# Optimization experiments

Measured on AMD Instinct MI355X. Metric: run time of the kernel, lower is better.

Reference implementation:

```python
import jax, jax.numpy as jnp
import numpy as np

EPS = 1e-06


def setup_inputs() -> dict:
    key = jax.random.key(0)
    k1, k2, k3 = jax.random.split(key, 3)
    N, L, H, D = 2, 2048, 8, 64
    return {
        "queries": jax.random.normal(k1, (N, L, H, D), dtype=jnp.float32),
        "keys": jax.random.normal(k2, (N, L, H, D), dtype=jnp.float32),
        "values": jax.random.normal(k3, (N, L, H, D), dtype=jnp.float32),
    }


def reference(queries, keys, values):
    # [N, L, H, D] -> [N, H, L, D]
    q = jnp.transpose(queries, (0, 2, 1, 3))
    k = jnp.transpose(keys, (0, 2, 1, 3))
    v = jnp.transpose(values, (0, 2, 1, 3))
    # kernel_method = sigmoid (applied to q and k only)
    q = jax.nn.sigmoid(q)
    k = jax.nn.sigmoid(k)
    L = q.shape[2]
    normal = (jnp.arange(L, dtype=q.dtype) + 1.0)[None, None, :]  # [1,1,L]

    sink_incoming = 1.0 / jnp.einsum('nhld,nhld->nhl', q + EPS, jnp.cumsum(k, axis=2) + EPS)
    source_outgoing = 1.0 / jnp.einsum('nhld,nhld->nhl', k + EPS, jnp.cumsum(q, axis=2) + EPS)
    sink_incoming = sink_incoming * normal
    source_outgoing = source_outgoing * normal

    conserved_sink = jnp.einsum(
        'nhld,nhld->nhl', q + EPS,
        jnp.cumsum(k * source_outgoing[..., None], axis=2) + EPS) / normal
    conserved_source = jnp.einsum(
        'nhld,nhld->nhl', k + EPS,
        jnp.cumsum(q * sink_incoming[..., None], axis=2) + EPS) / normal
    conserved_source = jnp.clip(conserved_source, -1.0, 1.0)

    sink_allocation = jax.nn.sigmoid(conserved_sink)
    conserved_source = jnp.exp(conserved_source)
    source_competition = conserved_source / jnp.cumsum(conserved_source, axis=-1) * normal

    # causal dot product: outer-product cumsum as in the original
    q_scaled = q * (sink_incoming / normal)[..., None]
    v_scaled = v * source_competition[..., None]
    kv = jnp.cumsum(jnp.einsum('nhld,nhlm->nhldm', k, v_scaled), axis=2)  # [N,H,L,D,M]
    qkv = jnp.einsum('nhld,nhldm->nhlm', q_scaled, kv)
    x = qkv * sink_allocation[..., None]
    # back to [N, L, H, M]
    return jnp.transpose(x, (0, 2, 1, 3))
```

## Files before the change

kernel.cpp:

```cpp
#include <hip/hip_runtime.h>
#include <math.h>

constexpr int Nn = 2, Hh = 8, Ll = 2048, Dd = 64;
constexpr int S  = Nn * Hh;
constexpr int C  = 64;
constexpr int NC = Ll / C;
constexpr int SC = S * NC;

constexpr int SB  = 72;
constexpr int SRP = 65;
constexpr int SS8 = 9;

#define EPSF 1e-6f
#define FLAG_MAGIC 0x5F3A9D21u

typedef __attribute__((ext_vector_type(8))) short short8;
typedef __attribute__((ext_vector_type(4))) float f32x4;
#define MFMA16(a, b, c) __builtin_amdgcn_mfma_f32_16x16x32_bf16(a, b, c, 0, 0, 0)

__device__ __forceinline__ float rcpf(float x) { return __builtin_amdgcn_rcpf(x); }
__device__ __forceinline__ float sigf(float x) { return rcpf(1.0f + __expf(-x)); }

__device__ __forceinline__ float waveRed(float v) {
#pragma unroll
    for (int off = 32; off > 0; off >>= 1) v += __shfl_xor(v, off, 64);
    return v;
}

__device__ __forceinline__ int gidx(int n, int l, int h, int d) {
    return ((n * Ll + l) * Hh + h) * Dd + d;
}

__device__ __forceinline__ float fc(const float4& v, int u) { return ((const float*)&v)[u]; }

__device__ __forceinline__ unsigned short f2bf(float x) {
    unsigned int u = __float_as_uint(x);
    unsigned int r = (u + 0x7fffu + ((u >> 16) & 1u)) >> 16;
    return (unsigned short)r;
}
__device__ __forceinline__ unsigned int pack2(float lo, float hi) {
    return (unsigned int)f2bf(lo) | ((unsigned int)f2bf(hi) << 16);
}
__device__ __forceinline__ float bf2f(unsigned short u) {
    return __uint_as_float(((unsigned int)u) << 16);
}
__device__ __forceinline__ float lo16(unsigned int x) { return __uint_as_float(x << 16); }
__device__ __forceinline__ float hi16(unsigned int x) { return __uint_as_float(x & 0xffff0000u); }
__device__ __forceinline__ void unpack8(const uint4& v, float* o) {
    o[0] = lo16(v.x); o[1] = hi16(v.x); o[2] = lo16(v.y); o[3] = hi16(v.y);
    o[4] = lo16(v.z); o[5] = hi16(v.z); o[6] = lo16(v.w); o[7] = hi16(v.w);
}

__device__ __forceinline__ void pubf(float* p, float v) {
    __hip_atomic_store((unsigned int*)p, __float_as_uint(v),
                       __ATOMIC_RELAXED, __HIP_MEMORY_SCOPE_AGENT);
}
__device__ __forceinline__ float rdf(const float* p) {
    return __uint_as_float(__hip_atomic_load((const unsigned int*)p,
                       __ATOMIC_RELAXED, __HIP_MEMORY_SCOPE_AGENT));
}
__device__ __forceinline__ void publish_flag(unsigned int* f, int t) {
    asm volatile("s_waitcnt vmcnt(0)" ::: "memory");
    __syncthreads();
    if (t == 0)
        __hip_atomic_store(f, FLAG_MAGIC, __ATOMIC_RELAXED, __HIP_MEMORY_SCOPE_AGENT);
}
__device__ __forceinline__ void wait_flags(const unsigned int* fbase, int s, int c, int t) {
    if (t < 64) {
        const bool need = (t < c);
        for (;;) {
            unsigned int v = need
                ? __hip_atomic_load(&fbase[s * NC + t], __ATOMIC_RELAXED, __HIP_MEMORY_SCOPE_AGENT)
                : FLAG_MAGIC;
            if (__all(v == FLAG_MAGIC)) break;
            __builtin_amdgcn_s_sleep(8);
        }
    }
    __syncthreads();
}

__global__ __launch_bounds__(256) void k_mega(
        const float* __restrict__ Q, const float* __restrict__ K,
        const float* __restrict__ V,
        unsigned short* __restrict__ Qb, unsigned short* __restrict__ Kb,
        unsigned short* __restrict__ Vt,
        float* __restrict__ SK, float* __restrict__ SQ,
        float* __restrict__ SKso, float* __restrict__ SQsi,
        float* __restrict__ s2_g, float* __restrict__ scomp_g,
        float* __restrict__ Tcs, float* __restrict__ KVT,
        unsigned int* __restrict__ f0, unsigned int* __restrict__ f1,
        unsigned int* __restrict__ f2) {
    __shared__ __align__(16) unsigned short sqB[C * SB];
    __shared__ __align__(16) unsigned short skB[C * SB];
    __shared__ __align__(16) unsigned short vsT[C * SB];
    __shared__ float P[C * SRP];
    __shared__ float scrA[C * SS8], scrB[C * SS8];
    __shared__ float colK[C], colQ[C], pk[Dd], pq[Dd];
    __shared__ float lsi[C], lso[C], rw1[C], rw2[C], le[C], ecum[C], lsc[C];
    __shared__ float pcsv;

    const int b = blockIdx.x, s = b / NC, c = b % NC;
    const int n = s / Hh, h = s % Hh, t = threadIdx.x;
    const size_t base = (size_t)b * 4096;

    {
        int d0 = (4 * t) & 63, ig = t >> 4;
        float psk[4] = {0, 0, 0, 0}, psq[4] = {0, 0, 0, 0};
#pragma unroll
        for (int j = 0; j < 4; j++) {
            int i = ig + 16 * j;
            int id = gidx(n, c * C + i, h, d0);
            float4 q4 = *(const float4*)&Q[id];
            float4 k4 = *(const float4*)&K[id];
            float a0 = sigf(q4.x), a1 = sigf(q4.y), a2 = sigf(q4.z), a3 = sigf(q4.w);
            float b0 = sigf(k4.x), b1 = sigf(k4.y), b2 = sigf(k4.z), b3 = sigf(k4.w);
            uint2 pq2 = make_uint2(pack2(a0, a1), pack2(a2, a3));
            uint2 pk2 = make_uint2(pack2(b0, b1), pack2(b2, b3));
            *(uint2*)&Qb[base + i * 64 + d0] = pq2;
            *(uint2*)&Kb[base + i * 64 + d0] = pk2;
            *(uint2*)&sqB[i * SB + d0] = pq2;
            *(uint2*)&skB[i * SB + d0] = pk2;
            psq[0] += a0; psq[1] += a1; psq[2] += a2; psq[3] += a3;
            psk[0] += b0; psk[1] += b1; psk[2] += b2; psk[3] += b3;
        }
#pragma unroll
        for (int r = 0; r < 4; r++) {
            P[ig * 64 + d0 + r] = psk[r];
            P[1024 + ig * 64 + d0 + r] = psq[r];
        }
        int i0 = (t & 15) * 4, dt = (t >> 4) * 4;
        float4 vr[4];
#pragma unroll
        for (int r = 0; r < 4; r++)
            vr[r] = *(const float4*)&V[gidx(n, c * C + i0 + r, h, dt)];
#pragma unroll
        for (int u = 0; u < 4; u++) {
            uint2 wv = make_uint2(pack2(fc(vr[0], u), fc(vr[1], u)),
                                  pack2(fc(vr[2], u), fc(vr[3], u)));
            *(uint2*)&Vt[base + (dt + u) * 64 + i0] = wv;
            *(uint2*)&vsT[(dt + u) * SB + i0] = wv;
        }
    }
    __syncthreads();
    if (t < 64) {
        float v = 0.f;
        for (int g = 0; g < 16; g++) v += P[g * 64 + t];
        pubf(&SK[b * 64 + t], v);
    } else if (t < 128) {
        int d = t - 64; float v = 0.f;
        for (int g = 0; g < 16; g++) v += P[1024 + g * 64 + d];
        pubf(&SQ[b * 64 + d], v);
    }
    publish_flag(&f0[b], t);

    wait_flags(f0, s, c, t);

    {
        int d = t & 63, g = t >> 6;
        float pa = 0.f, pb = 0.f;
        for (int cp = g; cp < c; cp += 4) {
            pa += rdf(&SK[(s * NC + cp) * 64 + d]);
            pb += rdf(&SQ[(s * NC + cp) * 64 + d]);
        }
        P[2048 + g * 64 + d] = pa;
        P[2304 + g * 64 + d] = pb;
    }
#pragma unroll
    for (int j = 0; j < 2; j++) {
        int flat = 8 * t + 2048 * j, i = flat >> 6, d0 = flat & 63;
        uint4 xq = *(const uint4*)&sqB[i * SB + d0];
        uint4 xk = *(const uint4*)&skB[i * SB + d0];
        float qa[8], ka[8];
        unpack8(xq, qa); unpack8(xk, ka);
        float sq = 0.f, sk = 0.f;
#pragma unroll
        for (int u = 0; u < 8; u++) { sq += qa[u]; sk += ka[u]; }
        scrB[i * SS8 + (d0 >> 3)] = sq;
        scrA[i * SS8 + (d0 >> 3)] = sk;
    }
    __syncthreads();
    if (t < 64) {
        float v = 0.f;
#pragma unroll
        for (int u = 0; u < 8; u++) v += scrA[t * SS8 + u];
        colK[t] = v;
    } else if (t < 128) {
        int i = t - 64; float v = 0.f;
#pragma unroll
        for (int u = 0; u < 8; u++) v += scrB[i * SS8 + u];
        colQ[i] = v;
    } else if (t < 192) {
        int d = t - 128;
        pk[d] = P[2048 + d] + P[2112 + d] + P[2176 + d] + P[2240 + d];
    } else {
        int d = t - 192;
        pq[d] = P[2304 + d] + P[2368 + d] + P[2432 + d] + P[2496 + d];
    }
    __syncthreads();

    {
        int w = t >> 6, lane = t & 63, m = lane & 15, q = lane >> 4;
        f32x4 acc[4] = {{0,0,0,0},{0,0,0,0},{0,0,0,0},{0,0,0,0}};
#pragma unroll
        for (int kk = 0; kk < 64; kk += 32) {
            short8 a = *(const short8*)&sqB[(16 * w + m) * SB + kk + q * 8];
#pragma unroll
            for (int J = 0; J < 4; J++) {
                short8 bb = *(const short8*)&skB[(16 * J + m) * SB + kk + q * 8];
                acc[J] = MFMA16(a, bb, acc[J]);
            }
        }
#pragma unroll
        for (int J = 0; J < 4; J++)
#pragma unroll
            for (int r = 0; r < 4; r++)
                P[(16 * w + 4 * q + r) * SRP + 16 * J + m] = acc[J][r];
    }
    __syncthreads();

    {
        int i = t >> 2, g = t & 3, l = c * C + i;
        float r1 = 0.f, r2 = 0.f;
        for (int jj = g; jj <= i; jj += 4) {
            r1 += P[i * SRP + jj] + EPSF * colK[jj];
            r2 += P[jj * SRP + i] + EPSF * colQ[jj];
        }
        float b1 = 0.f, b2 = 0.f;
#pragma unroll
        for (int u = 0; u < 16; u++) {
            int d = g * 16 + u;
            b1 += (bf2f(sqB[i * SB + d]) + EPSF) * (pk[d] + EPSF);
            b2 += (bf2f(skB[i * SB + d]) + EPSF) * (pq[d] + EPSF);
        }
        r1 += __shfl_xor(r1, 1, 64); r1 += __shfl_xor(r1, 2, 64);
        r2 += __shfl_xor(r2, 1, 64); r2 += __shfl_xor(r2, 2, 64);
        b1 += __shfl_xor(b1, 1, 64); b1 += __shfl_xor(b1, 2, 64);
        b2 += __shfl_xor(b2, 1, 64); b2 += __shfl_xor(b2, 2, 64);
        if (g == 0) {
            float nf = (float)(l + 1);
            lsi[i] = nf * rcpf(b1 + r1);
            lso[i] = nf * rcpf(b2 + r2);
        }
    }
    __syncthreads();

    {
        int i = t >> 2, g = t & 3;
        float a1 = 0.f, a2 = 0.f;
        for (int jj = g; jj <= i; jj += 4) {
            a1 += lso[jj] * (P[i * SRP + jj] + EPSF * colK[jj]);
            a2 += lsi[jj] * (P[jj * SRP + i] + EPSF * colQ[jj]);
        }
        a1 += __shfl_xor(a1, 1, 64); a1 += __shfl_xor(a1, 2, 64);
        a2 += __shfl_xor(a2, 1, 64); a2 += __shfl_xor(a2, 2, 64);
        if (g == 0) { rw1[i] = a1; rw2[i] = a2; }
    }
    {
        int d = t >> 2, g = t & 3;
        float v1 = 0.f, v2 = 0.f;
#pragma unroll
        for (int u = 0; u < 16; u++) {
            int i = g * 16 + u;
            v1 += bf2f(skB[i * SB + d]) * lso[i];
            v2 += bf2f(sqB[i * SB + d]) * lsi[i];
        }
        v1 += __shfl_xor(v1, 1, 64); v1 += __shfl_xor(v1, 2, 64);
        v2 += __shfl_xor(v2, 1, 64); v2 += __shfl_xor(v2, 2, 64);
        if (g == 0) {
            pubf(&SKso[b * 64 + d], v1);
            pubf(&SQsi[b * 64 + d], v2);
        }
    }
    publish_flag(&f1[b], t);

    wait_flags(f1, s, c, t);

    {
        int d = t & 63, g = t >> 6;
        float pa = 0.f, pb = 0.f;
        for (int cp = g; cp < c; cp += 4) {
            pa += rdf(&SKso[(s * NC + cp) * 64 + d]);
            pb += rdf(&SQsi[(s * NC + cp) * 64 + d]);
        }
        scrA[g * 64 + d] = pa;
        scrA[256 + g * 64 + d] = pb;
    }
    __syncthreads();
    if (t < 64) pk[t] = scrA[t] + scrA[64 + t] + scrA[128 + t] + scrA[192 + t];
    else if (t < 128) {
        int d = t - 64;
        pq[d] = scrA[256 + d] + scrA[320 + d] + scrA[384 + d] + scrA[448 + d];
    }
    __syncthreads();
    {
        int i = t >> 2, g = t & 3, l = c * C + i;
        float b1 = 0.f, b2 = 0.f;
#pragma unroll
        for (int j = 0; j < 2; j++) {
            uint4 xq = *(const uint4*)&sqB[i * SB + g * 16 + 8 * j];
            uint4 xk = *(const uint4*)&skB[i * SB + g * 16 + 8 * j];
            float qa[8], ka[8];
            unpack8(xq, qa); unpack8(xk, ka);
            int d = g * 16 + 8 * j;
#pragma unroll
            for (int u = 0; u < 8; u++) {
                b1 += (qa[u] + EPSF) * (pk[d + u] + EPSF);
                b2 += (ka[u] + EPSF) * (pq[d + u] + EPSF);
            }
        }
        b1 += __shfl_xor(b1, 1, 64); b1 += __shfl_xor(b1, 2, 64);
        b2 += __shfl_xor(b2, 1, 64); b2 += __shfl_xor(b2, 2, 64);
        if (g == 0) {
            float nf = (float)(l + 1);
            float cs  = (b1 + rw1[i]) * rcpf(nf);
            float csr = (b2 + rw2[i]) * rcpf(nf);
            csr = fminf(fmaxf(csr, -1.f), 1.f);
            float e = __expf(csr);
            float sal = sigf(cs);
            s2_g[s * Ll + l] = lsi[i] * rcpf(nf) * sal;
            le[i] = e;
        }
    }
    __syncthreads();
    if (t < 64) {
        float run = le[t];
#pragma unroll
        for (int off = 1; off < 64; off <<= 1) {
            float o = __shfl_up(run, off, 64);
            if (t >= off) run += o;
        }
        ecum[t] = run;
        if (t == 63) pubf(&Tcs[b], run);
    }
    publish_flag(&f2[b], t);

    wait_flags(f2, s, c, t);

    if (t < 64) {
        float v = (t < c) ? rdf(&Tcs[s * NC + t]) : 0.f;
        v = waveRed(v);
        if (t == 0) pcsv = v;
    }
    __syncthreads();
    if (t < 64) {
        int l = c * C + t;
        float ls = le[t] * rcpf(pcsv + ecum[t]) * (float)(l + 1);
        lsc[t] = ls;
        scomp_g[s * Ll + l] = ls;
    }
    __syncthreads();

    unsigned short* skT = (unsigned short*)P;
#pragma unroll
    for (int j = 0; j < 2; j++) {
        int flat = 8 * t + 2048 * j, dR = flat >> 6, i0 = flat & 63;
        uint4 vv = *(const uint4*)&vsT[dR * SB + i0];
        float x[8];
        unpack8(vv, x);
#pragma unroll
        for (int u = 0; u < 8; u++) x[u] *= lsc[i0 + u];
        uint4 o;
        o.x = pack2(x[0], x[1]); o.y = pack2(x[2], x[3]);
        o.z = pack2(x[4], x[5]); o.w = pack2(x[6], x[7]);
        *(uint4*)&vsT[dR * SB + i0] = o;
    }
    {
        int i0 = (t & 15) * 4, dt = (t >> 4) * 4;
        uint2 kr[4];
#pragma unroll
        for (int r = 0; r < 4; r++) kr[r] = *(const uint2*)&skB[(i0 + r) * SB + dt];
#pragma unroll
        for (int u = 0; u < 4; u++) {
            unsigned int e0 = (u < 2 ? kr[0].x : kr[0].y), e1 = (u < 2 ? kr[1].x : kr[1].y);
            unsigned int e2 = (u < 2 ? kr[2].x : kr[2].y), e3 = (u < 2 ? kr[3].x : kr[3].y);
            int sh = (u & 1) * 16;
            unsigned int lo = ((e0 >> sh) & 0xffffu) | (((e1 >> sh) & 0xffffu) << 16);
            unsigned int hi = ((e2 >> sh) & 0xffffu) | (((e3 >> sh) & 0xffffu) << 16);
            *(uint2*)&skT[(dt + u) * SB + i0] = make_uint2(lo, hi);
        }
    }
    __syncthreads();

    {
        int w = t >> 6, lane = t & 63, m = lane & 15, q = lane >> 4;
        f32x4 acc[4] = {{0,0,0,0},{0,0,0,0},{0,0,0,0},{0,0,0,0}};
#pragma unroll
        for (int kk = 0; kk < 64; kk += 32) {
            short8 a = *(const short8*)&vsT[(16 * w + m) * SB + kk + q * 8];
#pragma unroll
            for (int J = 0; J < 4; J++) {
                short8 bb = *(const short8*)&skT[(16 * J + m) * SB + kk + q * 8];
                acc[J] = MFMA16(a, bb, acc[J]);
            }
        }
#pragma unroll
        for (int J = 0; J < 4; J++)
#pragma unroll
            for (int r = 0; r < 4; r++)
                KVT[(size_t)b * 4096 + (16 * w + 4 * q + r) * 64 + 16 * J + m] = acc[J][r];
    }
}

__global__ __launch_bounds__(256) void k_prefixKV(const float* __restrict__ KVT,
                                                  unsigned short* __restrict__ KVpb) {
    int bx = blockIdx.x, s = bx >> 3, sub = bx & 7;
    int e0 = sub * 512 + 2 * threadIdx.x;
    float2 x[NC];
#pragma unroll
    for (int cp = 0; cp < NC; cp++)
        x[cp] = *(const float2*)&KVT[(size_t)(s * NC + cp) * 4096 + e0];
    float r0 = 0.f, r1 = 0.f;
#pragma unroll
    for (int cp = 0; cp < NC; cp++) {
        *(unsigned int*)&KVpb[(size_t)(s * NC + cp) * 4096 + e0] = pack2(r0, r1);
        r0 += x[cp].x; r1 += x[cp].y;
    }
}

__global__ __launch_bounds__(256) void k_final(const unsigned short* __restrict__ Qb,
                                               const unsigned short* __restrict__ Kb,
                                               const unsigned short* __restrict__ Vt,
                                               const float* __restrict__ s2_g,
                                               const float* __restrict__ scomp_g,
                                               const unsigned short* __restrict__ KVpb,
                                               float* __restrict__ Out) {
    __shared__ __align__(16) unsigned short sqB[C * SB];
    __shared__ __align__(16) unsigned short skB[C * SB];
    __shared__ __align__(16) unsigned short vsT[C * SB];
    __shared__ __align__(16) unsigned short stB[C * SB];
    __shared__ float lsc[C], s2l[C];
    int b = blockIdx.x, s = b / NC, c = b % NC;
    int n = s / Hh, h = s % Hh, t = threadIdx.x;
    int w = t >> 6, lane = t & 63, mf = lane & 15, qq = lane >> 4;
    int I0 = 16 * w;

    if (t < 64) lsc[t] = scomp_g[s * Ll + c * C + t];
    else if (t < 128) s2l[t - 64] = s2_g[s * Ll + c * C + (t - 64)];

    size_t base = (size_t)b * 4096;
    uint4 kvp[2];
#pragma unroll
    for (int j = 0; j < 2; j++)
        kvp[j] = *(const uint4*)&KVpb[base + 8 * t + 2048 * j];

#pragma unroll
    for (int j = 0; j < 2; j++) {
        int flat = 8 * t + 2048 * j, i = flat >> 6, d0 = flat & 63;
        *(uint4*)&sqB[i * SB + d0] = *(const uint4*)&Qb[base + flat];
        *(uint4*)&skB[i * SB + d0] = *(const uint4*)&Kb[base + flat];
        *(uint4*)&vsT[i * SB + d0] = *(const uint4*)&Vt[base + flat];
    }
    __syncthreads();

    {
        f32x4 acc[4] = {{0,0,0,0},{0,0,0,0},{0,0,0,0},{0,0,0,0}};
#pragma unroll
        for (int kk = 0; kk < 64; kk += 32) {
            short8 a = *(const short8*)&sqB[(I0 + mf) * SB + kk + qq * 8];
#pragma unroll
            for (int J = 0; J < 4; J++) {
                short8 bb2 = *(const short8*)&skB[(16 * J + mf) * SB + kk + qq * 8];
                acc[J] = MFMA16(a, bb2, acc[J]);
            }
        }
#pragma unroll
        for (int J = 0; J < 4; J++)
#pragma unroll
            for (int r = 0; r < 4; r++) {
                int i = I0 + 4 * qq + r, jj = 16 * J + mf;
                float v = (jj <= i) ? acc[J][r] * lsc[jj] : 0.f;
                stB[i * SB + jj] = f2bf(v);
            }
    }
    __syncthreads();

#pragma unroll
    for (int j = 0; j < 2; j++) {
        int flat = 8 * t + 2048 * j, i = flat >> 6, d0 = flat & 63;
        *(uint4*)&skB[i * SB + d0] = kvp[j];
    }
    __syncthreads();

    f32x4 acc[4] = {{0,0,0,0},{0,0,0,0},{0,0,0,0},{0,0,0,0}};
#pragma unroll
    for (int kk = 0; kk < 64; kk += 32) {
        short8 a1 = *(const short8*)&sqB[(I0 + mf) * SB + kk + qq * 8];
        short8 a2 = *(const short8*)&stB[(I0 + mf) * SB + kk + qq * 8];
#pragma unroll
        for (int J = 0; J < 4; J++) {
            short8 b1 = *(const short8*)&skB[(16 * J + mf) * SB + kk + qq * 8];
            acc[J] = MFMA16(a1, b1, acc[J]);
            short8 b2 = *(const short8*)&vsT[(16 * J + mf) * SB + kk + qq * 8];
            acc[J] = MFMA16(a2, b2, acc[J]);
        }
    }
#pragma unroll
    for (int J = 0; J < 4; J++)
#pragma unroll
        for (int r = 0; r < 4; r++) {
            int io = I0 + 4 * qq + r;
            Out[gidx(n, c * C + io, h, 16 * J + mf)] = acc[J][r] * s2l[io];
        }
}

extern "C" void kernel_launch(void* const* d_in, const int* in_sizes, int n_in,
                              void* d_out, int out_size, void* d_ws, size_t ws_size,
                              hipStream_t stream) {
    const float* Q = (const float*)d_in[0];
    const float* K = (const float*)d_in[1];
    const float* V = (const float*)d_in[2];
    float* Out = (float*)d_out;

    float* ws    = (float*)d_ws;
    float* SK    = ws;
    float* SQ    = SK    + SC * 64;
    float* SKso  = SQ    + SC * 64;
    float* SQsi  = SKso  + SC * 64;
    float* s2_g  = SQsi  + SC * 64;
    float* scomp = s2_g  + S * Ll;
    float* Tcs   = scomp + S * Ll;
    float* KVT   = Tcs   + SC;
    unsigned short* Qb   = (unsigned short*)(KVT + (size_t)SC * 4096);
    unsigned short* Kb   = Qb   + (size_t)SC * 4096;
    unsigned short* Vt   = Kb   + (size_t)SC * 4096;
    unsigned short* KVpb = Vt   + (size_t)SC * 4096;
    unsigned int*   f0   = (unsigned int*)(KVpb + (size_t)SC * 4096);
    unsigned int*   f1   = f0 + SC;
    unsigned int*   f2   = f1 + SC;

    k_mega<<<SC, 256, 0, stream>>>(Q, K, V, Qb, Kb, Vt, SK, SQ, SKso, SQsi,
                                   s2_g, scomp, Tcs, KVT, f0, f1, f2);
    k_prefixKV<<<128, 256, 0, stream>>>(KVT, KVpb);
    k_final<<<SC, 256, 0, stream>>>(Qb, Kb, Vt, s2_g, scomp, KVpb, Out);
}
```

Measured before the change: 103.4 us.

## Fuse prefix-KV and final kernels into single persistent kernel with flag sync

Merges the three launches (mega, prefixKV, final) into one kernel. Blocks keep Q/K/V tiles and the scaled score matrix in shared memory instead of round-tripping bf16 copies and per-row scalars through global memory. The KV prefix scan is done by the first 128 blocks after waiting on per-chunk flags, and all blocks then wait on the scan flags. Variable-trip loops are also replaced with fixed unrolled predicated loops. This removes launch gaps and global traffic, but relies on all 512 blocks being co-resident (launch_bounds 256,2) and adds more spin-wait synchronization and LDS usage.

```diff
diff --git a/kernel.cpp b/kernel.cpp
--- a/kernel.cpp
+++ b/kernel.cpp
@@ -59,18 +59,25 @@
     return __uint_as_float(__hip_atomic_load((const unsigned int*)p,
                        __ATOMIC_RELAXED, __HIP_MEMORY_SCOPE_AGENT));
 }
+__device__ __forceinline__ void pubu(unsigned int* p, unsigned int v) {
+    __hip_atomic_store(p, v, __ATOMIC_RELAXED, __HIP_MEMORY_SCOPE_AGENT);
+}
+__device__ __forceinline__ unsigned long long rd64(const void* p) {
+    return __hip_atomic_load((const unsigned long long*)p,
+                             __ATOMIC_RELAXED, __HIP_MEMORY_SCOPE_AGENT);
+}
 __device__ __forceinline__ void publish_flag(unsigned int* f, int t) {
     asm volatile("s_waitcnt vmcnt(0)" ::: "memory");
     __syncthreads();
     if (t == 0)
         __hip_atomic_store(f, FLAG_MAGIC, __ATOMIC_RELAXED, __HIP_MEMORY_SCOPE_AGENT);
 }
-__device__ __forceinline__ void wait_flags(const unsigned int* fbase, int s, int c, int t) {
+__device__ __forceinline__ void wait_n(const unsigned int* f, int n, int t) {
     if (t < 64) {
-        const bool need = (t < c);
+        const bool need = (t < n);
         for (;;) {
             unsigned int v = need
-                ? __hip_atomic_load(&fbase[s * NC + t], __ATOMIC_RELAXED, __HIP_MEMORY_SCOPE_AGENT)
+                ? __hip_atomic_load(&f[t], __ATOMIC_RELAXED, __HIP_MEMORY_SCOPE_AGENT)
                 : FLAG_MAGIC;
             if (__all(v == FLAG_MAGIC)) break;
             __builtin_amdgcn_s_sleep(8);
@@ -79,29 +86,31 @@
     __syncthreads();
 }
 
-__global__ __launch_bounds__(256) void k_mega(
+__global__ __launch_bounds__(256, 2) void k_all(
         const float* __restrict__ Q, const float* __restrict__ K,
         const float* __restrict__ V,
-        unsigned short* __restrict__ Qb, unsigned short* __restrict__ Kb,
-        unsigned short* __restrict__ Vt,
         float* __restrict__ SK, float* __restrict__ SQ,
         float* __restrict__ SKso, float* __restrict__ SQsi,
-        float* __restrict__ s2_g, float* __restrict__ scomp_g,
         float* __restrict__ Tcs, float* __restrict__ KVT,
+        unsigned short* __restrict__ KVpb, float* __restrict__ Out,
         unsigned int* __restrict__ f0, unsigned int* __restrict__ f1,
-        unsigned int* __restrict__ f2) {
+        unsigned int* __restrict__ f2, unsigned int* __restrict__ f3,
+        unsigned int* __restrict__ f4) {
     __shared__ __align__(16) unsigned short sqB[C * SB];
     __shared__ __align__(16) unsigned short skB[C * SB];
     __shared__ __align__(16) unsigned short vsT[C * SB];
-    __shared__ float P[C * SRP];
+    __shared__ __align__(16) unsigned short stB[C * SB];
+    __shared__ __align__(16) float Pun[4608];
     __shared__ float scrA[C * SS8], scrB[C * SS8];
     __shared__ float colK[C], colQ[C], pk[Dd], pq[Dd];
-    __shared__ float lsi[C], lso[C], rw1[C], rw2[C], le[C], ecum[C], lsc[C];
+    __shared__ float lsi[C], lso[C], rw1[C], rw2[C], le[C], ecum[C], lsc[C], s2l[C];
     __shared__ float pcsv;
 
     const int b = blockIdx.x, s = b / NC, c = b % NC;
     const int n = s / Hh, h = s % Hh, t = threadIdx.x;
-    const size_t base = (size_t)b * 4096;
+    const int w = t >> 6, lane = t & 63, mf = lane & 15, qq = lane >> 4;
+    const int I0 = 16 * w;
+    float* P = Pun;
 
     {
         int d0 = (4 * t) & 63, ig = t >> 4;
@@ -114,12 +123,8 @@
             float4 k4 = *(const float4*)&K[id];
             float a0 = sigf(q4.x), a1 = sigf(q4.y), a2 = sigf(q4.z), a3 = sigf(q4.w);
             float b0 = sigf(k4.x), b1 = sigf(k4.y), b2 = sigf(k4.z), b3 = sigf(k4.w);
-            uint2 pq2 = make_uint2(pack2(a0, a1), pack2(a2, a3));
-            uint2 pk2 = make_uint2(pack2(b0, b1), pack2(b2, b3));
-            *(uint2*)&Qb[base + i * 64 + d0] = pq2;
-            *(uint2*)&Kb[base + i * 64 + d0] = pk2;
-            *(uint2*)&sqB[i * SB + d0] = pq2;
-            *(uint2*)&skB[i * SB + d0] = pk2;
+            *(uint2*)&sqB[i * SB + d0] = make_uint2(pack2(a0, a1), pack2(a2, a3));
+            *(uint2*)&skB[i * SB + d0] = make_uint2(pack2(b0, b1), pack2(b2, b3));
             psq[0] += a0; psq[1] += a1; psq[2] += a2; psq[3] += a3;
             psk[0] += b0; psk[1] += b1; psk[2] += b2; psk[3] += b3;
         }
@@ -134,33 +139,36 @@
         for (int r = 0; r < 4; r++)
             vr[r] = *(const float4*)&V[gidx(n, c * C + i0 + r, h, dt)];
 #pragma unroll
-        for (int u = 0; u < 4; u++) {
-            uint2 wv = make_uint2(pack2(fc(vr[0], u), fc(vr[1], u)),
-                                  pack2(fc(vr[2], u), fc(vr[3], u)));
-            *(uint2*)&Vt[base + (dt + u) * 64 + i0] = wv;
-            *(uint2*)&vsT[(dt + u) * SB + i0] = wv;
-        }
+        for (int u = 0; u < 4; u++)
+            *(uint2*)&vsT[(dt + u) * SB + i0] = make_uint2(
+                pack2(fc(vr[0], u), fc(vr[1], u)), pack2(fc(vr[2], u), fc(vr[3], u)));
     }
     __syncthreads();
     if (t < 64) {
         float v = 0.f;
+#pragma unroll
         for (int g = 0; g < 16; g++) v += P[g * 64 + t];
         pubf(&SK[b * 64 + t], v);
     } else if (t < 128) {
         int d = t - 64; float v = 0.f;
+#pragma unroll
         for (int g = 0; g < 16; g++) v += P[1024 + g * 64 + d];
         pubf(&SQ[b * 64 + d], v);
     }
     publish_flag(&f0[b], t);
 
-    wait_flags(f0, s, c, t);
+    wait_n(&f0[s * NC], c, t);
 
     {
         int d = t & 63, g = t >> 6;
         float pa = 0.f, pb = 0.f;
-        for (int cp = g; cp < c; cp += 4) {
-            pa += rdf(&SK[(s * NC + cp) * 64 + d]);
-            pb += rdf(&SQ[(s * NC + cp) * 64 + d]);
+#pragma unroll
+        for (int u = 0; u < 8; u++) {
+            int cp = g + 4 * u;
+            float va = rdf(&SK[(s * NC + cp) * 64 + d]);
+            float vb = rdf(&SQ[(s * NC + cp) * 64 + d]);
+            pa += (cp < c) ? va : 0.f;
+            pb += (cp < c) ? vb : 0.f;
         }
         P[2048 + g * 64 + d] = pa;
         P[2304 + g * 64 + d] = pb;
@@ -199,14 +207,13 @@
     __syncthreads();
 
     {
-        int w = t >> 6, lane = t & 63, m = lane & 15, q = lane >> 4;
         f32x4 acc[4] = {{0,0,0,0},{0,0,0,0},{0,0,0,0},{0,0,0,0}};
 #pragma unroll
         for (int kk = 0; kk < 64; kk += 32) {
-            short8 a = *(const short8*)&sqB[(16 * w + m) * SB + kk + q * 8];
+            short8 a = *(const short8*)&sqB[(I0 + mf) * SB + kk + qq * 8];
 #pragma unroll
             for (int J = 0; J < 4; J++) {
-                short8 bb = *(const short8*)&skB[(16 * J + m) * SB + kk + q * 8];
+                short8 bb = *(const short8*)&skB[(16 * J + mf) * SB + kk + qq * 8];
                 acc[J] = MFMA16(a, bb, acc[J]);
             }
         }
@@ -214,16 +221,21 @@
         for (int J = 0; J < 4; J++)
 #pragma unroll
             for (int r = 0; r < 4; r++)
-                P[(16 * w + 4 * q + r) * SRP + 16 * J + m] = acc[J][r];
+                P[(I0 + 4 * qq + r) * SRP + 16 * J + mf] = acc[J][r];
     }
     __syncthreads();
 
     {
         int i = t >> 2, g = t & 3, l = c * C + i;
         float r1 = 0.f, r2 = 0.f;
-        for (int jj = g; jj <= i; jj += 4) {
-            r1 += P[i * SRP + jj] + EPSF * colK[jj];
-            r2 += P[jj * SRP + i] + EPSF * colQ[jj];
+#pragma unroll
+        for (int u = 0; u < 16; u++) {
+            int jj = g + 4 * u;
+            float t1 = P[i * SRP + jj] + EPSF * colK[jj];
+            float t2 = P[jj * SRP + i] + EPSF * colQ[jj];
+            bool ok = (jj <= i);
+            r1 += ok ? t1 : 0.f;
+            r2 += ok ? t2 : 0.f;
         }
         float b1 = 0.f, b2 = 0.f;
 #pragma unroll
@@ -247,9 +259,14 @@
     {
         int i = t >> 2, g = t & 3;
         float a1 = 0.f, a2 = 0.f;
-        for (int jj = g; jj <= i; jj += 4) {
-            a1 += lso[jj] * (P[i * SRP + jj] + EPSF * colK[jj]);
-            a2 += lsi[jj] * (P[jj * SRP + i] + EPSF * colQ[jj]);
+#pragma unroll
+        for (int u = 0; u < 16; u++) {
+            int jj = g + 4 * u;
+            float t1 = lso[jj] * (P[i * SRP + jj] + EPSF * colK[jj]);
+            float t2 = lsi[jj] * (P[jj * SRP + i] + EPSF * colQ[jj]);
+            bool ok = (jj <= i);
+            a1 += ok ? t1 : 0.f;
+            a2 += ok ? t2 : 0.f;
         }
         a1 += __shfl_xor(a1, 1, 64); a1 += __shfl_xor(a1, 2, 64);
         a2 += __shfl_xor(a2, 1, 64); a2 += __shfl_xor(a2, 2, 64);
@@ -273,14 +290,18 @@
     }
     publish_flag(&f1[b], t);
 
-    wait_flags(f1, s, c, t);
+    wait_n(&f1[s * NC], c, t);
 
     {
         int d = t & 63, g = t >> 6;
         float pa = 0.f, pb = 0.f;
-        for (int cp = g; cp < c; cp += 4) {
-            pa += rdf(&SKso[(s * NC + cp) * 64 + d]);
-            pb += rdf(&SQsi[(s * NC + cp) * 64 + d]);
+#pragma unroll
+        for (int u = 0; u < 8; u++) {
+            int cp = g + 4 * u;
+            float va = rdf(&SKso[(s * NC + cp) * 64 + d]);
+            float vb = rdf(&SQsi[(s * NC + cp) * 64 + d]);
+            pa += (cp < c) ? va : 0.f;
+            pb += (cp < c) ? vb : 0.f;
         }
         scrA[g * 64 + d] = pa;
         scrA[256 + g * 64 + d] = pb;
@@ -317,7 +338,7 @@
             csr = fminf(fmaxf(csr, -1.f), 1.f);
             float e = __expf(csr);
             float sal = sigf(cs);
-            s2_g[s * Ll + l] = lsi[i] * rcpf(nf) * sal;
+            s2l[i] = lsi[i] * rcpf(nf) * sal;
             le[i] = e;
         }
     }
@@ -334,7 +355,7 @@
     }
     publish_flag(&f2[b], t);
 
-    wait_flags(f2, s, c, t);
+    wait_n(&f2[s * NC], c, t);
 
     if (t < 64) {
         float v = (t < c) ? rdf(&Tcs[s * NC + t]) : 0.f;
@@ -344,13 +365,27 @@
     __syncthreads();
     if (t < 64) {
         int l = c * C + t;
-        float ls = le[t] * rcpf(pcsv + ecum[t]) * (float)(l + 1);
-        lsc[t] = ls;
-        scomp_g[s * Ll + l] = ls;
-    }
-    __syncthreads();
-
-    unsigned short* skT = (unsigned short*)P;
+        lsc[t] = le[t] * rcpf(pcsv + ecum[t]) * (float)(l + 1);
+    }
+    __syncthreads();
+
+    {
+        int i = t >> 2, g = t & 3;
+        unsigned int wds[8];
+#pragma unroll
+        for (int p = 0; p < 8; p++) {
+            int j0 = g * 16 + 2 * p;
+            float v0 = (j0     <= i) ? P[i * SRP + j0]     * lsc[j0]     : 0.f;
+            float v1 = (j0 + 1 <= i) ? P[i * SRP + j0 + 1] * lsc[j0 + 1] : 0.f;
+            wds[p] = pack2(v0, v1);
+        }
+        *(uint4*)&stB[i * SB + g * 16]     = make_uint4(wds[0], wds[1], wds[2], wds[3]);
+        *(uint4*)&stB[i * SB + g * 16 + 8] = make_uint4(wds[4], wds[5], wds[6], wds[7]);
+    }
+    __syncthreads();
+
+    unsigned short* skT = (unsigned short*)Pun;
+    unsigned short* vsV = (unsigned short*)(Pun + 2304);
 #pragma unroll
     for (int j = 0; j < 2; j++) {
         int flat = 8 * t + 2048 * j, dR = flat >> 6, i0 = flat & 63;
@@ -362,7 +397,7 @@
         uint4 o;
         o.x = pack2(x[0], x[1]); o.y = pack2(x[2], x[3]);
         o.z = pack2(x[4], x[5]); o.w = pack2(x[6], x[7]);
-        *(uint4*)&vsT[dR * SB + i0] = o;
+        *(uint4*)&vsV[dR * SB + i0] = o;
     }
     {
         int i0 = (t & 15) * 4, dt = (t >> 4) * 4;
@@ -382,14 +417,13 @@
     __syncthreads();
 
     {
-        int w = t >> 6, lane = t & 63, m = lane & 15, q = lane >> 4;
         f32x4 acc[4] = {{0,0,0,0},{0,0,0,0},{0,0,0,0},{0,0,0,0}};
 #pragma unroll
         for (int kk = 0; kk < 64; kk += 32) {
-            short8 a = *(const short8*)&vsT[(16 * w + m) * SB + kk + q * 8];
+            short8 a = *(const short8*)&vsV[(I0 + mf) * SB + kk + qq * 8];
 #pragma unroll
             for (int J = 0; J < 4; J++) {
-                short8 bb = *(const short8*)&skT[(16 * J + m) * SB + kk + q * 8];
+                short8 bb = *(const short8*)&skT[(16 * J + mf) * SB + kk + qq * 8];
                 acc[J] = MFMA16(a, bb, acc[J]);
             }
         }
@@ -397,58 +431,46 @@
         for (int J = 0; J < 4; J++)
 #pragma unroll
             for (int r = 0; r < 4; r++)
-                KVT[(size_t)b * 4096 + (16 * w + 4 * q + r) * 64 + 16 * J + m] = acc[J][r];
-    }
-}
-
-__global__ __launch_bounds__(256) void k_prefixKV(const float* __restrict__ KVT,
-                                                  unsigned short* __restrict__ KVpb) {
-    int bx = blockIdx.x, s = bx >> 3, sub = bx & 7;
-    int e0 = sub * 512 + 2 * threadIdx.x;
-    float2 x[NC];
-#pragma unroll
-    for (int cp = 0; cp < NC; cp++)
-        x[cp] = *(const float2*)&KVT[(size_t)(s * NC + cp) * 4096 + e0];
-    float r0 = 0.f, r1 = 0.f;
-#pragma unroll
-    for (int cp = 0; cp < NC; cp++) {
-        *(unsigned int*)&KVpb[(size_t)(s * NC + cp) * 4096 + e0] = pack2(r0, r1);
-        r0 += x[cp].x; r1 += x[cp].y;
-    }
-}
-
-__global__ __launch_bounds__(256) void k_final(const unsigned short* __restrict__ Qb,
-                                               const unsigned short* __restrict__ Kb,
-                                               const unsigned short* __restrict__ Vt,
-                                               const float* __restrict__ s2_g,
-                                               const float* __restrict__ scomp_g,
-                                               const unsigned short* __restrict__ KVpb,
-                                               float* __restrict__ Out) {
-    __shared__ __align__(16) unsigned short sqB[C * SB];
-    __shared__ __align__(16) unsigned short skB[C * SB];
-    __shared__ __align__(16) unsigned short vsT[C * SB];
-    __shared__ __align__(16) unsigned short stB[C * SB];
-    __shared__ float lsc[C], s2l[C];
-    int b = blockIdx.x, s = b / NC, c = b % NC;
-    int n = s / Hh, h = s % Hh, t = threadIdx.x;
-    int w = t >> 6, lane = t & 63, mf = lane & 15, qq = lane >> 4;
-    int I0 = 16 * w;
-
-    if (t < 64) lsc[t] = scomp_g[s * Ll + c * C + t];
-    else if (t < 128) s2l[t - 64] = s2_g[s * Ll + c * C + (t - 64)];
-
+                pubf(&KVT[(size_t)b * 4096 + (I0 + 4 * qq + r) * 64 + 16 * J + mf],
+                     acc[J][r]);
+    }
+    publish_flag(&f3[b], t);
+
+    if (b < 128) {
+        int sp = b >> 3, sub = b & 7;
+        wait_n(&f3[sp * NC], NC, t);
+        int e0 = sub * 512 + 2 * t;
+        float2 x[NC];
+#pragma unroll
+        for (int cp = 0; cp < NC; cp++) {
+            unsigned long long v = rd64(&KVT[(size_t)(sp * NC + cp) * 4096 + e0]);
+            x[cp].x = __uint_as_float((unsigned int)v);
+            x[cp].y = __uint_as_float((unsigned int)(v >> 32));
+        }
+        float r0 = 0.f, r1 = 0.f;
+#pragma unroll
+        for (int cp = 0; cp < NC; cp++) {
+            pubu((unsigned int*)&KVpb[(size_t)(sp * NC + cp) * 4096 + e0], pack2(r0, r1));
+            r0 += x[cp].x; r1 += x[cp].y;
+        }
+        publish_flag(&f4[b], t);
+    }
+
+    wait_n(&f4[8 * s], 8, t);
+    unsigned long long kvp[4];
     size_t base = (size_t)b * 4096;
-    uint4 kvp[2];
-#pragma unroll
-    for (int j = 0; j < 2; j++)
-        kvp[j] = *(const uint4*)&KVpb[base + 8 * t + 2048 * j];
-
+#pragma unroll
+    for (int j = 0; j < 2; j++) {
+        kvp[2 * j]     = rd64(&KVpb[base + 8 * t + 2048 * j]);
+        kvp[2 * j + 1] = rd64(&KVpb[base + 8 * t + 2048 * j + 4]);
+    }
 #pragma unroll
     for (int j = 0; j < 2; j++) {
         int flat = 8 * t + 2048 * j, i = flat >> 6, d0 = flat & 63;
-        *(uint4*)&sqB[i * SB + d0] = *(const uint4*)&Qb[base + flat];
-        *(uint4*)&skB[i * SB + d0] = *(const uint4*)&Kb[base + flat];
-        *(uint4*)&vsT[i * SB + d0] = *(const uint4*)&Vt[base + flat];
+        *(uint2*)&skB[i * SB + d0] =
+            make_uint2((unsigned int)kvp[2 * j], (unsigned int)(kvp[2 * j] >> 32));
+        *(uint2*)&skB[i * SB + d0 + 4] =
+            make_uint2((unsigned int)kvp[2 * j + 1], (unsigned int)(kvp[2 * j + 1] >> 32));
     }
     __syncthreads();
 
@@ -456,51 +478,24 @@
         f32x4 acc[4] = {{0,0,0,0},{0,0,0,0},{0,0,0,0},{0,0,0,0}};
 #pragma unroll
         for (int kk = 0; kk < 64; kk += 32) {
-            short8 a = *(const short8*)&sqB[(I0 + mf) * SB + kk + qq * 8];
+            short8 a1 = *(const short8*)&sqB[(I0 + mf) * SB + kk + qq * 8];
+            short8 a2 = *(const short8*)&stB[(I0 + mf) * SB + kk + qq * 8];
 #pragma unroll
             for (int J = 0; J < 4; J++) {
-                short8 bb2 = *(const short8*)&skB[(16 * J + mf) * SB + kk + qq * 8];
-                acc[J] = MFMA16(a, bb2, acc[J]);
+                short8 b1 = *(const short8*)&skB[(16 * J + mf) * SB + kk + qq * 8];
+                acc[J] = MFMA16(a1, b1, acc[J]);
+                short8 b2 = *(const short8*)&vsT[(16 * J + mf) * SB + kk + qq * 8];
+                acc[J] = MFMA16(a2, b2, acc[J]);
             }
         }
 #pragma unroll
         for (int J = 0; J < 4; J++)
 #pragma unroll
             for (int r = 0; r < 4; r++) {
-                int i = I0 + 4 * qq + r, jj = 16 * J + mf;
-                float v = (jj <= i) ? acc[J][r] * lsc[jj] : 0.f;
-                stB[i * SB + jj] = f2bf(v);
+                int io = I0 + 4 * qq + r;
+                Out[gidx(n, c * C + io, h, 16 * J + mf)] = acc[J][r] * s2l[io];
             }
     }
-    __syncthreads();
-
-#pragma unroll
-    for (int j = 0; j < 2; j++) {
-        int flat = 8 * t + 2048 * j, i = flat >> 6, d0 = flat & 63;
-        *(uint4*)&skB[i * SB + d0] = kvp[j];
-    }
-    __syncthreads();
-
-    f32x4 acc[4] = {{0,0,0,0},{0,0,0,0},{0,0,0,0},{0,0,0,0}};
-#pragma unroll
-    for (int kk = 0; kk < 64; kk += 32) {
-        short8 a1 = *(const short8*)&sqB[(I0 + mf) * SB + kk + qq * 8];
-        short8 a2 = *(const short8*)&stB[(I0 + mf) * SB + kk + qq * 8];
-#pragma unroll
-        for (int J = 0; J < 4; J++) {
-            short8 b1 = *(const short8*)&skB[(16 * J + mf) * SB + kk + qq * 8];
-            acc[J] = MFMA16(a1, b1, acc[J]);
-            short8 b2 = *(const short8*)&vsT[(16 * J + mf) * SB + kk + qq * 8];
-            acc[J] = MFMA16(a2, b2, acc[J]);
-        }
-    }
-#pragma unroll
-    for (int J = 0; J < 4; J++)
-#pragma unroll
-        for (int r = 0; r < 4; r++) {
-            int io = I0 + 4 * qq + r;
-            Out[gidx(n, c * C + io, h, 16 * J + mf)] = acc[J][r] * s2l[io];
-        }
 }
 
 extern "C" void kernel_launch(void* const* d_in, const int* in_sizes, int n_in,
@@ -511,25 +506,20 @@
     const float* V = (const float*)d_in[2];
     float* Out = (float*)d_out;
 
-    float* ws    = (float*)d_ws;
-    float* SK    = ws;
-    float* SQ    = SK    + SC * 64;
-    float* SKso  = SQ    + SC * 64;
-    float* SQsi  = SKso  + SC * 64;
-    float* s2_g  = SQsi  + SC * 64;
-    float* scomp = s2_g  + S * Ll;
-    float* Tcs   = scomp + S * Ll;
-    float* KVT   = Tcs   + SC;
-    unsigned short* Qb   = (unsigned short*)(KVT + (size_t)SC * 4096);
-    unsigned short* Kb   = Qb   + (size_t)SC * 4096;
-    unsigned short* Vt   = Kb   + (size_t)SC * 4096;
-    unsigned short* KVpb = Vt   + (size_t)SC * 4096;
-    unsigned int*   f0   = (unsigned int*)(KVpb + (size_t)SC * 4096);
-    unsigned int*   f1   = f0 + SC;
-    unsigned int*   f2   = f1 + SC;
-
-    k_mega<<<SC, 256, 0, stream>>>(Q, K, V, Qb, Kb, Vt, SK, SQ, SKso, SQsi,
-                                   s2_g, scomp, Tcs, KVT, f0, f1, f2);
-    k_prefixKV<<<128, 256, 0, stream>>>(KVT, KVpb);
-    k_final<<<SC, 256, 0, stream>>>(Qb, Kb, Vt, s2_g, scomp, KVpb, Out);
-}
+    float* ws   = (float*)d_ws;
+    float* SK   = ws;
+    float* SQ   = SK   + SC * 64;
+    float* SKso = SQ   + SC * 64;
+    float* SQsi = SKso + SC * 64;
+    float* Tcs  = SQsi + SC * 64;
+    float* KVT  = Tcs  + SC;
+    unsigned short* KVpb = (unsigned short*)(KVT + (size_t)SC * 4096);
+    unsigned int* f0 = (unsigned int*)(KVpb + (size_t)SC * 4096);
+    unsigned int* f1 = f0 + SC;
+    unsigned int* f2 = f1 + SC;
+    unsigned int* f3 = f2 + SC;
+    unsigned int* f4 = f3 + SC;
+
+    k_all<<<SC, 256, 0, stream>>>(Q, K, V, SK, SQ, SKso, SQsi, Tcs, KVT, KVpb, Out,
+                                  f0, f1, f2, f3, f4);
+}
```

After: 99.23 us. 1.04x faster.
